# Optimization experiments

Hardware: AMD Instinct MI355X
Metric: run time of the kernel (lower is better)

The kernel has to match this reference:

```python
import jax, jax.numpy as jnp
import numpy as np

SPARSITY_RATIO = 0.1


def setup_inputs() -> dict:
    key = jax.random.key(0)
    ks = jax.random.split(key, 11)
    B, S, d = 4, 2048, 16  # d = n_sparse_dims + 2
    inp = {
        "full": jax.random.normal(ks[0], (B, S, d), dtype=jnp.float32),
        "sw1": jax.random.normal(ks[1], (d, 32), dtype=jnp.float32) * 0.1,
        "sb1": jax.random.normal(ks[2], (32,), dtype=jnp.float32) * 0.1,
        "sw2": jax.random.normal(ks[3], (32, 1), dtype=jnp.float32) * 0.1,
        "sb2": jax.random.normal(ks[4], (1,), dtype=jnp.float32) * 0.1,
        "mw1": jax.random.normal(ks[5], (3 * d, 64), dtype=jnp.float32) * 0.1,
        "mb1": jax.random.normal(ks[6], (64,), dtype=jnp.float32) * 0.1,
        "mw2": jax.random.normal(ks[7], (64, 32), dtype=jnp.float32) * 0.1,
        "mb2": jax.random.normal(ks[8], (32,), dtype=jnp.float32) * 0.1,
        "mw3": jax.random.normal(ks[9], (32, d), dtype=jnp.float32) * 0.1,
        "mb3": jax.random.normal(ks[10], (d,), dtype=jnp.float32) * 0.1,
    }
    return inp


def reference(full, sw1, sb1, sw2, sb2, mw1, mb1, mw2, mb2, mw3, mb3):
    B, S, d = full.shape
    k = max(1, int(S * SPARSITY_RATIO))  # static python int

    # importance scores: Linear(d,32) -> ReLU -> Linear(32,1)
    scores = (jax.nn.relu(full @ sw1 + sb1) @ sw2 + sb2)[..., 0]  # [B, S]
    _, top_idx = jax.lax.top_k(scores, k)  # [B, k]

    # gather selected tokens (keys == values)
    sel = jnp.take_along_axis(full, top_idx[:, :, None], axis=1)  # [B, k, d]

    # First MLP layer on concat([q, keys, values]) decomposed to avoid the
    # [B,S,k,3d] concat: mw1 splits into query / key / value blocks.
    w_q, w_k, w_v = mw1[:d], mw1[d:2 * d], mw1[2 * d:]
    q_part = full @ w_q                     # [B, S, 64]
    kv_part = sel @ (w_k + w_v)             # [B, k, 64]
    h1 = jax.nn.relu(q_part[:, :, None, :] + kv_part[:, None, :, :] + mb1)  # [B,S,k,64]
    h2 = jax.nn.relu(h1 @ mw2 + mb2)        # [B, S, k, 32]
    out = h2 @ mw3 + mb3                    # [B, S, k, d]
    return out.mean(axis=2)                 # [B, S, d]
```

## Files before the change

kernel.cpp:

```cpp
#include <hip/hip_runtime.h>
#include <hip/hip_bf16.h>

#define BB 4
#define SS 2048
#define DD 16
#define KK 204
#define JSPLIT 8

typedef __attribute__((ext_vector_type(8))) short short8;
typedef __attribute__((ext_vector_type(4))) float f32x4;

__device__ inline short f2bf(float x) {
  __hip_bfloat16 b = __float2bfloat16(x);
  return *reinterpret_cast<short*>(&b);
}

__global__ void __launch_bounds__(256) score_q_kernel(
    const float* __restrict__ full, const float* __restrict__ sw1,
    const float* __restrict__ sb1, const float* __restrict__ sw2,
    const float* __restrict__ sb2, const float* __restrict__ mw1,
    float* __restrict__ scores, float* __restrict__ qpart) {
  int idx = blockIdx.x * blockDim.x + threadIdx.x;
  if (idx >= BB * SS) return;
  float x[16];
  const float* xp = full + idx * DD;
#pragma unroll
  for (int i = 0; i < 16; i++) x[i] = xp[i];

  float sc = sb2[0];
#pragma unroll
  for (int n = 0; n < 32; n++) {
    float a = sb1[n];
#pragma unroll
    for (int k = 0; k < 16; k++) a += x[k] * sw1[k * 32 + n];
    a = fmaxf(a, 0.f);
    sc += a * sw2[n];
  }
  scores[idx] = sc;

#pragma unroll
  for (int n = 0; n < 64; n++) {
    float a = 0.f;
#pragma unroll
    for (int k = 0; k < 16; k++) a += x[k] * mw1[k * 64 + n];
    qpart[idx * 64 + n] = a;
  }
}

__global__ void __launch_bounds__(256) topk_select_kernel(
    const float* __restrict__ scores, int* __restrict__ topidx) {
  int b = blockIdx.x;
  int t = threadIdx.x;

  unsigned long long key[8];
#pragma unroll
  for (int e = 0; e < 8; e++) {
    int i = t + e * 256;
    float f = scores[b * SS + i];
    unsigned u = __float_as_uint(f);
    u = (u & 0x80000000u) ? ~u : (u | 0x80000000u);
    key[e] = ((unsigned long long)u << 11) | (unsigned)(SS - 1 - i);
  }

  __shared__ int hist[256];
  __shared__ int sufs[256];
  __shared__ unsigned long long s_prefix;
  __shared__ int s_r;
  __shared__ int s_cnt;
  if (t == 0) { s_prefix = 0ull; s_r = KK; s_cnt = 0; }

  for (int s = 40; s >= 0; s -= 8) {
    hist[t] = 0;
    __syncthreads();
    unsigned long long pfx = s_prefix;
#pragma unroll
    for (int e = 0; e < 8; e++) {
      if ((key[e] >> (s + 8)) == pfx)
        atomicAdd(&hist[(int)((key[e] >> s) & 0xFF)], 1);
    }
    __syncthreads();
    sufs[t] = hist[t];
    __syncthreads();
    for (int off = 1; off < 256; off <<= 1) {
      int add = (t + off < 256) ? sufs[t + off] : 0;
      __syncthreads();
      sufs[t] += add;
      __syncthreads();
    }
    int r = s_r;
    int nxt = (t < 255) ? sufs[t + 1] : 0;
    if (sufs[t] >= r && nxt < r) {
      s_prefix = (pfx << 8) | (unsigned)t;
      s_r = r - nxt;
    }
    __syncthreads();
  }

  unsigned long long kstar = s_prefix;
#pragma unroll
  for (int e = 0; e < 8; e++) {
    if (key[e] >= kstar) {
      int pos = atomicAdd(&s_cnt, 1);
      topidx[b * KK + pos] = t + e * 256;
    }
  }
}

__global__ void __launch_bounds__(64) kvb_kernel(
    const float* __restrict__ full, const int* __restrict__ topidx,
    const float* __restrict__ mw1, const float* __restrict__ mb1,
    float* __restrict__ kvb) {
  int bj = blockIdx.x;
  int b = bj / KK, j = bj % KK;
  int n = threadIdx.x;
  __shared__ float x[16];
  int sidx = topidx[b * KK + j];
  if (n < 16) x[n] = full[(b * SS + sidx) * DD + n];
  __syncthreads();
  float a = mb1[n];
#pragma unroll
  for (int k = 0; k < 16; k++)
    a += x[k] * (mw1[(16 + k) * 64 + n] + mw1[(32 + k) * 64 + n]);
  kvb[(b * KK + j) * 64 + n] = a;
}

__global__ void __launch_bounds__(512) main_mfma_kernel(
    const float* __restrict__ qpart, const float* __restrict__ kvb,
    const float* __restrict__ mw2, const float* __restrict__ mb2,
    const float* __restrict__ mw3, const float* __restrict__ mb3,
    float* __restrict__ out) {
  int mtile = blockIdx.x;
  int bs_base = mtile * 16;
  int b = bs_base >> 11;
  int t = threadIdx.x;
  int w = t >> 6;
  int l = t & 63;
  int ml = l & 15;
  int g = l >> 4;

  f32x4 qv[2][2];
  {
    const float* qp = qpart + (bs_base + ml) * 64 + 8 * g;
    qv[0][0] = *(const f32x4*)(qp);
    qv[0][1] = *(const f32x4*)(qp + 4);
    qv[1][0] = *(const f32x4*)(qp + 32);
    qv[1][1] = *(const f32x4*)(qp + 36);
  }

  short8 bfrag[2][2];
#pragma unroll
  for (int nt = 0; nt < 2; nt++)
#pragma unroll
    for (int kh = 0; kh < 2; kh++)
#pragma unroll
      for (int i = 0; i < 8; i++) {
        int k = kh * 32 + 8 * g + i;
        bfrag[nt][kh][i] = f2bf(mw2[k * 32 + nt * 16 + ml]);
      }

  f32x4 biasfrag[2];
#pragma unroll
  for (int nt = 0; nt < 2; nt++) {
    float bv = mb2[nt * 16 + ml];
    f32x4 bf;
    bf[0] = bv; bf[1] = bv; bf[2] = bv; bf[3] = bv;
    biasfrag[nt] = bf;
  }

  float accs[2][4] = {};
  int jbeg = w * 26;
  int jend = jbeg + 26;
  if (jend > KK) jend = KK;
  const float* kvbb = kvb + b * KK * 64 + 8 * g;

#pragma unroll 2
  for (int j = jbeg; j < jend; j++) {
    const float* kp = kvbb + j * 64;
    f32x4 kv[2][2];
    kv[0][0] = *(const f32x4*)(kp);
    kv[0][1] = *(const f32x4*)(kp + 4);
    kv[1][0] = *(const f32x4*)(kp + 32);
    kv[1][1] = *(const f32x4*)(kp + 36);

    short8 afrag[2];
#pragma unroll
    for (int kh = 0; kh < 2; kh++)
#pragma unroll
      for (int hf = 0; hf < 2; hf++)
#pragma unroll
        for (int i = 0; i < 4; i++) {
          float h = fmaxf(qv[kh][hf][i] + kv[kh][hf][i], 0.f);
          afrag[kh][hf * 4 + i] = f2bf(h);
        }

#pragma unroll
    for (int nt = 0; nt < 2; nt++) {
      f32x4 c = __builtin_amdgcn_mfma_f32_16x16x32_bf16(
          afrag[0], bfrag[nt][0], biasfrag[nt], 0, 0, 0);
      c = __builtin_amdgcn_mfma_f32_16x16x32_bf16(
          afrag[1], bfrag[nt][1], c, 0, 0, 0);
#pragma unroll
      for (int r = 0; r < 4; r++) accs[nt][r] += fmaxf(c[r], 0.f);
    }
  }

  __shared__ float red[JSPLIT][512];
#pragma unroll
  for (int nt = 0; nt < 2; nt++)
#pragma unroll
    for (int r = 0; r < 4; r++)
      red[w][(4 * g + r) * 32 + nt * 16 + ml] = accs[nt][r];
  __syncthreads();
  float sum = 0.f;
#pragma unroll
  for (int ww = 0; ww < JSPLIT; ww++) sum += red[ww][t];
  sum *= (1.0f / (float)KK);
  red[0][t] = sum;
  __syncthreads();

  if (t < 256) {
    int m = t >> 4, dc = t & 15;
    float o = mb3[dc];
#pragma unroll
    for (int n = 0; n < 32; n++) o += red[0][m * 32 + n] * mw3[n * 16 + dc];
    out[(bs_base + m) * 16 + dc] = o;
  }
}

extern "C" void kernel_launch(void* const* d_in, const int* in_sizes, int n_in,
                              void* d_out, int out_size, void* d_ws, size_t ws_size,
                              hipStream_t stream) {
  const float* full = (const float*)d_in[0];
  const float* sw1  = (const float*)d_in[1];
  const float* sb1  = (const float*)d_in[2];
  const float* sw2  = (const float*)d_in[3];
  const float* sb2  = (const float*)d_in[4];
  const float* mw1  = (const float*)d_in[5];
  const float* mb1  = (const float*)d_in[6];
  const float* mw2  = (const float*)d_in[7];
  const float* mb2  = (const float*)d_in[8];
  const float* mw3  = (const float*)d_in[9];
  const float* mb3  = (const float*)d_in[10];
  float* out = (float*)d_out;

  float* ws = (float*)d_ws;
  float* scores = ws;
  float* qpart  = scores + BB * SS;
  float* kvb    = qpart + BB * SS * 64;
  int*   topidx = (int*)(kvb + BB * KK * 64);

  score_q_kernel<<<(BB * SS) / 256, 256, 0, stream>>>(full, sw1, sb1, sw2, sb2,
                                                      mw1, scores, qpart);
  topk_select_kernel<<<BB, 256, 0, stream>>>(scores, topidx);
  kvb_kernel<<<BB * KK, 64, 0, stream>>>(full, topidx, mw1, mb1, kvb);
  main_mfma_kernel<<<BB * SS / 16, 512, 0, stream>>>(qpart, kvb, mw2, mb2, mw3,
                                                     mb3, out);
}
```

Before: 45.19 us.

## Fuse top-k selection with KV projection and use 11-bit radix passes

Merges the top-k selection kernel and the per-selected-token KV projection kernel into one kernel per batch, removing a launch and the topidx round trip through global memory. The radix select now runs four 11-bit passes instead of six 8-bit passes, and the suffix sums use wave shuffles in place of a barrier-heavy shared-memory scan. Selected indices are compacted deterministically with a prefix scan instead of atomics. The KV projection is now done by only 4 blocks (one per batch), so it has far less parallelism than the previous 816-block launch. The main kernel's ReLU is vectorized, which is mostly cosmetic.

Result: slower. 49.61 us (+9.8%).

```diff
diff --git a/kernel.cpp b/kernel.cpp
--- a/kernel.cpp
+++ b/kernel.cpp
@@ -47,10 +47,26 @@
   }
 }
 
-__global__ void __launch_bounds__(256) topk_select_kernel(
-    const float* __restrict__ scores, int* __restrict__ topidx) {
+__global__ void __launch_bounds__(256) topk_kvb_kernel(
+    const float* __restrict__ scores, const float* __restrict__ full,
+    const float* __restrict__ mw1, const float* __restrict__ mb1,
+    float* __restrict__ kvb) {
   int b = blockIdx.x;
   int t = threadIdx.x;
+  int lane = t & 63, w = t >> 6;
+
+  __shared__ int hist[2048];
+  __shared__ int wtot[4];
+  __shared__ unsigned long long s_pfx;
+  __shared__ int s_r;
+  __shared__ int s_idx[KK];
+  __shared__ float wsum[16 * 64];
+
+#pragma unroll
+  for (int kk = 0; kk < 4; kk++) {
+    int k = kk * 4 + w;
+    wsum[k * 64 + lane] = mw1[(16 + k) * 64 + lane] + mw1[(32 + k) * 64 + lane];
+  }
 
   unsigned long long key[8];
 #pragma unroll
@@ -61,67 +77,95 @@
     u = (u & 0x80000000u) ? ~u : (u | 0x80000000u);
     key[e] = ((unsigned long long)u << 11) | (unsigned)(SS - 1 - i);
   }
-
-  __shared__ int hist[256];
-  __shared__ int sufs[256];
-  __shared__ unsigned long long s_prefix;
-  __shared__ int s_r;
-  __shared__ int s_cnt;
-  if (t == 0) { s_prefix = 0ull; s_r = KK; s_cnt = 0; }
-
-  for (int s = 40; s >= 0; s -= 8) {
-    hist[t] = 0;
+  if (t == 0) { s_pfx = 0ull; s_r = KK; }
+
+#pragma unroll
+  for (int pass = 0; pass < 4; pass++) {
+    int s = 33 - pass * 11;
+#pragma unroll
+    for (int z = 0; z < 8; z++) hist[t + z * 256] = 0;
     __syncthreads();
-    unsigned long long pfx = s_prefix;
+    unsigned long long pfx = s_pfx;
+    int r = s_r;
 #pragma unroll
     for (int e = 0; e < 8; e++) {
-      if ((key[e] >> (s + 8)) == pfx)
-        atomicAdd(&hist[(int)((key[e] >> s) & 0xFF)], 1);
+      if ((key[e] >> (s + 11)) == pfx)
+        atomicAdd(&hist[(int)((key[e] >> s) & 0x7FF)], 1);
     }
     __syncthreads();
-    sufs[t] = hist[t];
+    int loc[8], ls[9];
+#pragma unroll
+    for (int i = 0; i < 8; i++) loc[i] = hist[t * 8 + i];
+    ls[8] = 0;
+#pragma unroll
+    for (int i = 7; i >= 0; i--) ls[i] = ls[i + 1] + loc[i];
+    int tot = ls[0];
+    int incl = tot;
+#pragma unroll
+    for (int off = 1; off < 64; off <<= 1) {
+      int o = __shfl_down(incl, off);
+      incl += (lane + off < 64) ? o : 0;
+    }
+    if (lane == 0) wtot[w] = incl;
     __syncthreads();
-    for (int off = 1; off < 256; off <<= 1) {
-      int add = (t + off < 256) ? sufs[t + off] : 0;
-      __syncthreads();
-      sufs[t] += add;
-      __syncthreads();
-    }
-    int r = s_r;
-    int nxt = (t < 255) ? sufs[t + 1] : 0;
-    if (sufs[t] >= r && nxt < r) {
-      s_prefix = (pfx << 8) | (unsigned)t;
-      s_r = r - nxt;
+    int waveoff = 0;
+    for (int ww = w + 1; ww < 4; ww++) waveoff += wtot[ww];
+    int excl_thread = waveoff + (incl - tot);
+#pragma unroll
+    for (int i = 0; i < 8; i++) {
+      int sufs = ls[i] + excl_thread;
+      int sufn = ls[i + 1] + excl_thread;
+      if (sufs >= r && sufn < r) {
+        s_pfx = (pfx << 11) | (unsigned)(t * 8 + i);
+        s_r = r - sufn;
+      }
     }
     __syncthreads();
   }
 
-  unsigned long long kstar = s_prefix;
+  unsigned long long kstar = s_pfx;
+  bool selm[8];
+  int c = 0;
 #pragma unroll
   for (int e = 0; e < 8; e++) {
-    if (key[e] >= kstar) {
-      int pos = atomicAdd(&s_cnt, 1);
-      topidx[b * KK + pos] = t + e * 256;
-    }
-  }
-}
-
-__global__ void __launch_bounds__(64) kvb_kernel(
-    const float* __restrict__ full, const int* __restrict__ topidx,
-    const float* __restrict__ mw1, const float* __restrict__ mb1,
-    float* __restrict__ kvb) {
-  int bj = blockIdx.x;
-  int b = bj / KK, j = bj % KK;
-  int n = threadIdx.x;
-  __shared__ float x[16];
-  int sidx = topidx[b * KK + j];
-  if (n < 16) x[n] = full[(b * SS + sidx) * DD + n];
+    selm[e] = (key[e] >= kstar);
+    c += selm[e] ? 1 : 0;
+  }
+  int p = c;
+#pragma unroll
+  for (int off = 1; off < 64; off <<= 1) {
+    int o = __shfl_up(p, off);
+    p += (lane >= off) ? o : 0;
+  }
+  if (lane == 63) wtot[w] = p;
   __syncthreads();
-  float a = mb1[n];
-#pragma unroll
-  for (int k = 0; k < 16; k++)
-    a += x[k] * (mw1[(16 + k) * 64 + n] + mw1[(32 + k) * 64 + n]);
-  kvb[(b * KK + j) * 64 + n] = a;
+  int base = 0;
+  for (int ww = 0; ww < w; ww++) base += wtot[ww];
+  int pos = base + p - c;
+#pragma unroll
+  for (int e = 0; e < 8; e++) {
+    if (selm[e]) s_idx[pos++] = t + e * 256;
+  }
+  __syncthreads();
+
+  float biasv = mb1[lane];
+  for (int j = w; j < KK; j += 4) {
+    const float* xp = full + (b * SS + s_idx[j]) * DD;
+    f32x4 x0 = *(const f32x4*)(xp);
+    f32x4 x1 = *(const f32x4*)(xp + 4);
+    f32x4 x2 = *(const f32x4*)(xp + 8);
+    f32x4 x3 = *(const f32x4*)(xp + 12);
+    float a = biasv;
+#pragma unroll
+    for (int k = 0; k < 4; k++) a += x0[k] * wsum[k * 64 + lane];
+#pragma unroll
+    for (int k = 0; k < 4; k++) a += x1[k] * wsum[(4 + k) * 64 + lane];
+#pragma unroll
+    for (int k = 0; k < 4; k++) a += x2[k] * wsum[(8 + k) * 64 + lane];
+#pragma unroll
+    for (int k = 0; k < 4; k++) a += x3[k] * wsum[(12 + k) * 64 + lane];
+    kvb[(b * KK + j) * 64 + lane] = a;
+  }
 }
 
 __global__ void __launch_bounds__(512) main_mfma_kernel(
@@ -167,6 +211,7 @@
     biasfrag[nt] = bf;
   }
 
+  const f32x4 zero4 = {0.f, 0.f, 0.f, 0.f};
   float accs[2][4] = {};
   int jbeg = w * 26;
   int jend = jbeg + 26;
@@ -176,31 +221,31 @@
 #pragma unroll 2
   for (int j = jbeg; j < jend; j++) {
     const float* kp = kvbb + j * 64;
-    f32x4 kv[2][2];
-    kv[0][0] = *(const f32x4*)(kp);
-    kv[0][1] = *(const f32x4*)(kp + 4);
-    kv[1][0] = *(const f32x4*)(kp + 32);
-    kv[1][1] = *(const f32x4*)(kp + 36);
+    f32x4 kvv[2][2];
+    kvv[0][0] = *(const f32x4*)(kp);
+    kvv[0][1] = *(const f32x4*)(kp + 4);
+    kvv[1][0] = *(const f32x4*)(kp + 32);
+    kvv[1][1] = *(const f32x4*)(kp + 36);
 
     short8 afrag[2];
 #pragma unroll
     for (int kh = 0; kh < 2; kh++)
 #pragma unroll
-      for (int hf = 0; hf < 2; hf++)
-#pragma unroll
-        for (int i = 0; i < 4; i++) {
-          float h = fmaxf(qv[kh][hf][i] + kv[kh][hf][i], 0.f);
-          afrag[kh][hf * 4 + i] = f2bf(h);
-        }
+      for (int hf = 0; hf < 2; hf++) {
+        f32x4 s = qv[kh][hf] + kvv[kh][hf];
+        f32x4 r = __builtin_elementwise_max(s, zero4);
+#pragma unroll
+        for (int i = 0; i < 4; i++) afrag[kh][hf * 4 + i] = f2bf(r[i]);
+      }
 
 #pragma unroll
     for (int nt = 0; nt < 2; nt++) {
-      f32x4 c = __builtin_amdgcn_mfma_f32_16x16x32_bf16(
+      f32x4 cacc = __builtin_amdgcn_mfma_f32_16x16x32_bf16(
           afrag[0], bfrag[nt][0], biasfrag[nt], 0, 0, 0);
-      c = __builtin_amdgcn_mfma_f32_16x16x32_bf16(
-          afrag[1], bfrag[nt][1], c, 0, 0, 0);
-#pragma unroll
-      for (int r = 0; r < 4; r++) accs[nt][r] += fmaxf(c[r], 0.f);
+      cacc = __builtin_amdgcn_mfma_f32_16x16x32_bf16(
+          afrag[1], bfrag[nt][1], cacc, 0, 0, 0);
+#pragma unroll
+      for (int r = 0; r < 4; r++) accs[nt][r] += fmaxf(cacc[r], 0.f);
     }
   }
 
@@ -247,12 +292,10 @@
   float* scores = ws;
   float* qpart  = scores + BB * SS;
   float* kvb    = qpart + BB * SS * 64;
-  int*   topidx = (int*)(kvb + BB * KK * 64);
 
   score_q_kernel<<<(BB * SS) / 256, 256, 0, stream>>>(full, sw1, sb1, sw2, sb2,
                                                       mw1, scores, qpart);
-  topk_select_kernel<<<BB, 256, 0, stream>>>(scores, topidx);
-  kvb_kernel<<<BB * KK, 64, 0, stream>>>(full, topidx, mw1, mb1, kvb);
+  topk_kvb_kernel<<<BB, 256, 0, stream>>>(scores, full, mw1, mb1, kvb);
   main_mfma_kernel<<<BB * SS / 16, 512, 0, stream>>>(qpart, kvb, mw2, mb2, mw3,
                                                      mb3, out);
 }
```
